# Kernel optimization log

Hardware: AMD Instinct MI355X
Metric: run time of the kernel (lower is better)

## Reference

```python
import math
import jax, jax.numpy as jnp
import numpy as np

DIMS = 20
MULT = 8
K = (DIMS + 1) * MULT  # 168 mixture components
N = 524288
EPS = 1.0              # log_density default eps
BASE_COV = 0.1
LOG_NORM = -DIMS / 2 * math.log(2 * math.pi)


def setup_inputs() -> dict:
    key = jax.random.key(0)
    k1, k2, k3 = jax.random.split(key, 3)
    sample = jax.random.normal(k1, (N, DIMS), dtype=jnp.float32) * 0.3
    alpha = jax.random.normal(k2, (K,), dtype=jnp.float32) * 0.1
    mu = jax.random.uniform(k3, (K, DIMS), dtype=jnp.float32, minval=-0.5, maxval=0.5)
    cov = jnp.full((K, DIMS), BASE_COV, dtype=jnp.float32)
    return {"sample": sample, "alpha": alpha, "mu": mu, "cov": cov}


def reference(sample, alpha, mu, cov):
    # Faithful vectorization of the per-component Python loop in log_density.
    var = EPS ** 2
    weights = jax.nn.softmax(alpha)                       # [K]
    i = jnp.arange(K) // MULT                             # component group index, 0..DIMS
    d = jnp.arange(DIMS)
    # cov[:i] *= var  ->  scale first i dims of each component's cov by var
    scale = jnp.where(d[None, :] < i[:, None], var, 1.0)  # [K, D]
    inv = 1.0 / (cov * scale)                             # [K, D]
    # det_cov = var**i * (1/10)**(dims - i)  (exactly as in the source)
    fi = i.astype(jnp.float32)
    det_cov = var ** fi * BASE_COV ** (DIMS - fi)         # [K]
    sig_term = det_cov ** -0.5                            # [K]
    # quad[n,k] = sum_d (x[n,d]-mu[k,d])^2 * inv[k,d], expanded into GEMMs
    quad = (sample ** 2) @ inv.T \
           - 2.0 * (sample @ (mu * inv).T) \
           + jnp.sum(mu * mu * inv, axis=1)[None, :]      # [N, K]
    results = sig_term * jnp.exp(-0.5 * quad) * weights   # [N, K]
    density = results.sum(axis=1, keepdims=True)          # [N, 1]
    return jnp.log(density) + LOG_NORM
```

## Files before the change

kernel.cpp:

```cpp
#include <hip/hip_runtime.h>
#include <math.h>


#define DIMS     20
#define MULT     8
#define K_COMP   168
#define KC_PAD   176
#define BROW     72
#define BASE_COV 0.1f
#define LOG2E    1.4426950408889634f
#define LN2      0.6931471805599453f
#define LOG_NORM -18.378770664093453f
#define CPW      8
#define NB       1024

typedef _Float16 f16x8 __attribute__((ext_vector_type(8)));
typedef _Float16 f16x2 __attribute__((ext_vector_type(2)));
typedef float    f32x4 __attribute__((ext_vector_type(4)));
typedef unsigned int uint;
typedef uint u32x4 __attribute__((ext_vector_type(4)));

__device__ __forceinline__ uint pk(float lo, float hi) {
    return __builtin_bit_cast(uint, __builtin_amdgcn_cvt_pkrtz(lo, hi));
}
__device__ __forceinline__ uint pksq(uint a) {
    f16x2 v = __builtin_bit_cast(f16x2, a);
    return __builtin_bit_cast(uint, (f16x2)(v * v));
}

__global__ __launch_bounds__(256) void gm_fused(const float* __restrict__ sample,
                                                const float* __restrict__ alpha,
                                                const float* __restrict__ mu,
                                                const float* __restrict__ cov,
                                                float* __restrict__ out) {
    __shared__ __attribute__((aligned(16))) _Float16 lds_T[KC_PAD][BROW];
    __shared__ float sh_logZ;
    const int tid = threadIdx.x;

    uint* bz = (uint*)&lds_T[0][0];
    for (int i = tid; i < KC_PAD * BROW / 2; i += 256) bz[i] = 0u;
    __syncthreads();

    if (tid < 64) {
        float a0 = (tid       < K_COMP) ? alpha[tid]       : -1e30f;
        float a1 = (tid + 64  < K_COMP) ? alpha[tid + 64]  : -1e30f;
        float a2 = (tid + 128 < K_COMP) ? alpha[tid + 128] : -1e30f;
        float m = fmaxf(fmaxf(a0, a1), a2);
        for (int msk = 32; msk; msk >>= 1) m = fmaxf(m, __shfl_xor(m, msk, 64));
        float s = __expf(a0 - m) + __expf(a1 - m) + __expf(a2 - m);
        for (int msk = 32; msk; msk >>= 1) s += __shfl_xor(s, msk, 64);
        if (tid == 0) sh_logZ = m + __logf(s);
    }
    __syncthreads();

    if (tid < K_COMP) {
        const int   n  = tid;
        const int   i  = n / MULT;
        const float fi = (float)i;
        const float var = 1.0f;
        float logdet = fi * __logf(var) + ((float)DIMS - fi) * __logf(BASE_COV);
        const float4* cvp = (const float4*)(cov + n * DIMS);
        const float4* mup = (const float4*)(mu + n * DIMS);
        float4 c0 = cvp[0], c1 = cvp[1], c2 = cvp[2], c3 = cvp[3], c4 = cvp[4];
        float4 m0 = mup[0], m1 = mup[1], m2 = mup[2], m3 = mup[3], m4 = mup[4];
        float C = 0.0f;
        auto emit = [&](int d, float cc, float mm) {
            float scale = (d < i) ? var : 1.0f;
            float inv   = 1.0f / (cc * scale);
            C += mm * mm * inv;
            lds_T[n][d]        = (_Float16)(-0.5f * inv * LOG2E);
            lds_T[n][DIMS + d] = (_Float16)(mm * inv * LOG2E);
        };
        emit( 0, c0.x, m0.x); emit( 1, c0.y, m0.y); emit( 2, c0.z, m0.z); emit( 3, c0.w, m0.w);
        emit( 4, c1.x, m1.x); emit( 5, c1.y, m1.y); emit( 6, c1.z, m1.z); emit( 7, c1.w, m1.w);
        emit( 8, c2.x, m2.x); emit( 9, c2.y, m2.y); emit(10, c2.z, m2.z); emit(11, c2.w, m2.w);
        emit(12, c3.x, m3.x); emit(13, c3.y, m3.y); emit(14, c3.z, m3.z); emit(15, c3.w, m3.w);
        emit(16, c4.x, m4.x); emit(17, c4.y, m4.y); emit(18, c4.z, m4.z); emit(19, c4.w, m4.w);
        float L2 = ((alpha[n] - sh_logZ) - 0.5f * logdet - 0.5f * C) * LOG2E;
        lds_T[n][2 * DIMS] = (_Float16)L2;
    } else if (tid < KC_PAD) {
        lds_T[tid][2 * DIMS] = (_Float16)(-65504.0f);
    }
    __syncthreads();

    const int w = tid >> 6, l = tid & 63, q = l >> 4, c = l & 15;
    const bool qa = (q & 1) != 0, qb = (q & 2) != 0;
    const uint onezero = 0x00003C00u;
    const f32x4 zero = { 0.f, 0.f, 0.f, 0.f };
    const int base = blockIdx.x * (64 * CPW) + w * 16 + c;

#define MAKE_FRAGS(CC)                                                          \
    f16x8 sf1_##CC, sf2_##CC;                                                   \
    {                                                                           \
        const float4* rp = (const float4*)(sample + (size_t)(base + (CC) * 64) * DIMS); \
        float4 r0 = rp[0], r1 = rp[1], r2 = rp[2], r3 = rp[3], r4 = rp[4];      \
        uint q0 = pk(r0.x, r0.y), q1 = pk(r0.z, r0.w);                          \
        uint q2 = pk(r1.x, r1.y), q3 = pk(r1.z, r1.w);                          \
        uint q4 = pk(r2.x, r2.y), q5 = pk(r2.z, r2.w);                          \
        uint q6 = pk(r3.x, r3.y), q7 = pk(r3.z, r3.w);                          \
        uint q8 = pk(r4.x, r4.y), q9 = pk(r4.z, r4.w);                          \
        uint s0 = pksq(q0), s1 = pksq(q1), s2 = pksq(q2), s3 = pksq(q3);        \
        uint s4 = pksq(q4), s5 = pksq(q5), s6 = pksq(q6), s7 = pksq(q7);        \
        uint s8 = pksq(q8), s9 = pksq(q9);                                      \
        uint f1_0 = qb ? (qa ? q2 : s8) : (qa ? s4 : s0);                       \
        uint f1_1 = qb ? (qa ? q3 : s9) : (qa ? s5 : s1);                       \
        uint f1_2 = qb ? (qa ? q4 : q0) : (qa ? s6 : s2);                       \
        uint f1_3 = qb ? (qa ? q5 : q1) : (qa ? s7 : s3);                       \
        uint f2_0 = qb ? 0u : (qa ? onezero : q6);                              \
        uint f2_1 = qb ? 0u : (qa ? 0u : q7);                                   \
        uint f2_2 = qb ? 0u : (qa ? 0u : q8);                                   \
        uint f2_3 = qb ? 0u : (qa ? 0u : q9);                                   \
        u32x4 w1 = { f1_0, f1_1, f1_2, f1_3 };                                  \
        u32x4 w2 = { f2_0, f2_1, f2_2, f2_3 };                                  \
        sf1_##CC = __builtin_bit_cast(f16x8, w1);                               \
        sf2_##CC = __builtin_bit_cast(f16x8, w2);                               \
    }

    MAKE_FRAGS(0) MAKE_FRAGS(1) MAKE_FRAGS(2) MAKE_FRAGS(3)
    MAKE_FRAGS(4) MAKE_FRAGS(5) MAKE_FRAGS(6) MAKE_FRAGS(7)
#undef MAKE_FRAGS

    float d0 = 0.f, d1 = 0.f, d2 = 0.f, d3 = 0.f;
    float d4 = 0.f, d5 = 0.f, d6 = 0.f, d7 = 0.f;
#pragma unroll
    for (int t = 0; t < KC_PAD / 16; ++t) {
        f16x8 cf1 = *(const f16x8*)&lds_T[t * 16 + c][q * 8];
        f16x8 cf2 = *(const f16x8*)&lds_T[t * 16 + c][32 + q * 8];
#define DO_CHUNK(CC)                                                            \
        {                                                                       \
            f32x4 acc = __builtin_amdgcn_mfma_f32_16x16x32_f16(cf1, sf1_##CC, zero, 0, 0, 0); \
            acc       = __builtin_amdgcn_mfma_f32_16x16x32_f16(cf2, sf2_##CC, acc,  0, 0, 0); \
            d##CC += (__builtin_amdgcn_exp2f(acc[0]) + __builtin_amdgcn_exp2f(acc[1]))        \
                   + (__builtin_amdgcn_exp2f(acc[2]) + __builtin_amdgcn_exp2f(acc[3]));       \
        }
        DO_CHUNK(0) DO_CHUNK(1) DO_CHUNK(2) DO_CHUNK(3)
        DO_CHUNK(4) DO_CHUNK(5) DO_CHUNK(6) DO_CHUNK(7)
#undef DO_CHUNK
    }

    const int ob = blockIdx.x * (64 * CPW) + w * 16;
#define FINISH(CC, DD)                                                          \
    {                                                                           \
        float dn = DD;                                                          \
        dn += __shfl_xor(dn, 16, 64);                                           \
        dn += __shfl_xor(dn, 32, 64);                                           \
        if (l < 16) out[ob + (CC) * 64 + l] = LN2 * __builtin_amdgcn_logf(dn) + LOG_NORM; \
    }
    FINISH(0, d0) FINISH(1, d1) FINISH(2, d2) FINISH(3, d3)
    FINISH(4, d4) FINISH(5, d5) FINISH(6, d6) FINISH(7, d7)
#undef FINISH
}

extern "C" void kernel_launch(void* const* d_in, const int* in_sizes, int n_in,
                              void* d_out, int out_size, void* d_ws, size_t ws_size,
                              hipStream_t stream) {
    const float* sample = (const float*)d_in[0];
    const float* alpha  = (const float*)d_in[1];
    const float* mu     = (const float*)d_in[2];
    const float* cov    = (const float*)d_in[3];
    float* out = (float*)d_out;
    gm_fused<<<NB, 256, 0, stream>>>(sample, alpha, mu, cov, out);
}
```

Baseline: 115.4 us.

## Hoist component fragments into registers and stream sample chunks one at a time

Inverts the loop nest. All 11 component-tile fragments are now loaded from LDS once into registers, and each of the 8 sample chunks is loaded, multiplied against every tile, reduced and written out before the next chunk starts. This removes the repeated LDS reads per tile and the need to hold all 16 sample fragments at once. It also adds a launch-bounds occupancy hint of 3 blocks per CU. The trade-off is that the 22 fragment registers stay live for the whole loop, and sample loads are serialized per chunk instead of all issued up front, which may expose global load latency.

```diff
diff --git a/kernel.cpp b/kernel.cpp
--- a/kernel.cpp
+++ b/kernel.cpp
@@ -28,11 +28,11 @@
     return __builtin_bit_cast(uint, (f16x2)(v * v));
 }
 
-__global__ __launch_bounds__(256) void gm_fused(const float* __restrict__ sample,
-                                                const float* __restrict__ alpha,
-                                                const float* __restrict__ mu,
-                                                const float* __restrict__ cov,
-                                                float* __restrict__ out) {
+__global__ __launch_bounds__(256, 3) void gm_fused(const float* __restrict__ sample,
+                                                   const float* __restrict__ alpha,
+                                                   const float* __restrict__ mu,
+                                                   const float* __restrict__ cov,
+                                                   float* __restrict__ out) {
     __shared__ __attribute__((aligned(16))) _Float16 lds_T[KC_PAD][BROW];
     __shared__ float sh_logZ;
     const int tid = threadIdx.x;
@@ -87,12 +87,27 @@
     const bool qa = (q & 1) != 0, qb = (q & 2) != 0;
     const uint onezero = 0x00003C00u;
     const f32x4 zero = { 0.f, 0.f, 0.f, 0.f };
-    const int base = blockIdx.x * (64 * CPW) + w * 16 + c;
 
-#define MAKE_FRAGS(CC)                                                          \
-    f16x8 sf1_##CC, sf2_##CC;                                                   \
+#define LOAD_CF(T)                                                              \
+    const f16x8 cf1_##T = *(const f16x8*)&lds_T[(T) * 16 + c][q * 8];           \
+    const f16x8 cf2_##T = *(const f16x8*)&lds_T[(T) * 16 + c][32 + q * 8];
+    LOAD_CF(0) LOAD_CF(1) LOAD_CF(2) LOAD_CF(3) LOAD_CF(4) LOAD_CF(5)
+    LOAD_CF(6) LOAD_CF(7) LOAD_CF(8) LOAD_CF(9) LOAD_CF(10)
+#undef LOAD_CF
+
+    const int base = blockIdx.x * (64 * CPW) + w * 16;
+
+#define DO_TILE(T)                                                              \
+        {                                                                       \
+            f32x4 acc = __builtin_amdgcn_mfma_f32_16x16x32_f16(cf1_##T, sf1, zero, 0, 0, 0); \
+            acc       = __builtin_amdgcn_mfma_f32_16x16x32_f16(cf2_##T, sf2, acc,  0, 0, 0); \
+            dens += (__builtin_amdgcn_exp2f(acc[0]) + __builtin_amdgcn_exp2f(acc[1]))        \
+                  + (__builtin_amdgcn_exp2f(acc[2]) + __builtin_amdgcn_exp2f(acc[3]));       \
+        }
+
+#define DO_CHUNK(CC)                                                            \
     {                                                                           \
-        const float4* rp = (const float4*)(sample + (size_t)(base + (CC) * 64) * DIMS); \
+        const float4* rp = (const float4*)(sample + (size_t)(base + (CC) * 64 + c) * DIMS); \
         float4 r0 = rp[0], r1 = rp[1], r2 = rp[2], r3 = rp[3], r4 = rp[4];      \
         uint q0 = pk(r0.x, r0.y), q1 = pk(r0.z, r0.w);                          \
         uint q2 = pk(r1.x, r1.y), q3 = pk(r1.z, r1.w);                          \
@@ -112,43 +127,21 @@
         uint f2_3 = qb ? 0u : (qa ? 0u : q9);                                   \
         u32x4 w1 = { f1_0, f1_1, f1_2, f1_3 };                                  \
         u32x4 w2 = { f2_0, f2_1, f2_2, f2_3 };                                  \
-        sf1_##CC = __builtin_bit_cast(f16x8, w1);                               \
-        sf2_##CC = __builtin_bit_cast(f16x8, w2);                               \
+        f16x8 sf1 = __builtin_bit_cast(f16x8, w1);                              \
+        f16x8 sf2 = __builtin_bit_cast(f16x8, w2);                              \
+        float dens = 0.0f;                                                      \
+        DO_TILE(0) DO_TILE(1) DO_TILE(2) DO_TILE(3) DO_TILE(4) DO_TILE(5)       \
+        DO_TILE(6) DO_TILE(7) DO_TILE(8) DO_TILE(9) DO_TILE(10)                 \
+        dens += __shfl_xor(dens, 16, 64);                                       \
+        dens += __shfl_xor(dens, 32, 64);                                       \
+        if (l < 16)                                                             \
+            out[base + (CC) * 64 + l] = LN2 * __builtin_amdgcn_logf(dens) + LOG_NORM; \
     }
 
-    MAKE_FRAGS(0) MAKE_FRAGS(1) MAKE_FRAGS(2) MAKE_FRAGS(3)
-    MAKE_FRAGS(4) MAKE_FRAGS(5) MAKE_FRAGS(6) MAKE_FRAGS(7)
-#undef MAKE_FRAGS
-
-    float d0 = 0.f, d1 = 0.f, d2 = 0.f, d3 = 0.f;
-    float d4 = 0.f, d5 = 0.f, d6 = 0.f, d7 = 0.f;
-#pragma unroll
-    for (int t = 0; t < KC_PAD / 16; ++t) {
-        f16x8 cf1 = *(const f16x8*)&lds_T[t * 16 + c][q * 8];
-        f16x8 cf2 = *(const f16x8*)&lds_T[t * 16 + c][32 + q * 8];
-#define DO_CHUNK(CC)                                                            \
-        {                                                                       \
-            f32x4 acc = __builtin_amdgcn_mfma_f32_16x16x32_f16(cf1, sf1_##CC, zero, 0, 0, 0); \
-            acc       = __builtin_amdgcn_mfma_f32_16x16x32_f16(cf2, sf2_##CC, acc,  0, 0, 0); \
-            d##CC += (__builtin_amdgcn_exp2f(acc[0]) + __builtin_amdgcn_exp2f(acc[1]))        \
-                   + (__builtin_amdgcn_exp2f(acc[2]) + __builtin_amdgcn_exp2f(acc[3]));       \
-        }
-        DO_CHUNK(0) DO_CHUNK(1) DO_CHUNK(2) DO_CHUNK(3)
-        DO_CHUNK(4) DO_CHUNK(5) DO_CHUNK(6) DO_CHUNK(7)
+    DO_CHUNK(0) DO_CHUNK(1) DO_CHUNK(2) DO_CHUNK(3)
+    DO_CHUNK(4) DO_CHUNK(5) DO_CHUNK(6) DO_CHUNK(7)
 #undef DO_CHUNK
-    }
-
-    const int ob = blockIdx.x * (64 * CPW) + w * 16;
-#define FINISH(CC, DD)                                                          \
-    {                                                                           \
-        float dn = DD;                                                          \
-        dn += __shfl_xor(dn, 16, 64);                                           \
-        dn += __shfl_xor(dn, 32, 64);                                           \
-        if (l < 16) out[ob + (CC) * 64 + l] = LN2 * __builtin_amdgcn_logf(dn) + LOG_NORM; \
-    }
-    FINISH(0, d0) FINISH(1, d1) FINISH(2, d2) FINISH(3, d3)
-    FINISH(4, d4) FINISH(5, d5) FINISH(6, d6) FINISH(7, d7)
-#undef FINISH
+#undef DO_TILE
 }
 
 extern "C" void kernel_launch(void* const* d_in, const int* in_sizes, int n_in,
```

New measurement: 96.06 us. 16.8% less time.
